# Kernel optimization log

Measured on AMD Instinct MI355X. Metric: run time of the kernel, lower is better.

The kernel has to match this reference:

```python
import jax, jax.numpy as jnp
import numpy as np

WORD_THRES = 0.2
COS_EPS = 1e-8
NEG_INF = -1e9


def setup_inputs() -> dict:
    key = jax.random.key(0)
    k1, k2, k3, k4 = jax.random.split(key, 4)
    B, L, V, E, A = 1024, 256, 50000, 300, 30
    inputs = jax.random.randint(k1, (B, L), 0, V)            # token ids, 0 == pad
    w_emb = jax.random.normal(k2, (V, E), dtype=jnp.float32) * 0.1
    a_emb = jax.random.normal(k3, (A, E), dtype=jnp.float32)
    a_weight = jax.random.uniform(k4, (A,), dtype=jnp.float32)
    return {"inputs": inputs, "w_emb": w_emb, "a_emb": a_emb, "a_weight": a_weight}


def reference(inputs, w_emb, a_emb, a_weight):
    # inputs: [B, L] int ids; w_emb: [V, E]; a_emb: [A, E]; a_weight: [A]
    inputs_len = (inputs != 0).sum(axis=1).astype(jnp.float32)      # [B]
    x_wrd = w_emb[inputs]                                            # [B, L, E]

    # cosine similarity between each aspect and each word (torch semantics:
    # dot / (max(||a||, eps) * max(||x||, eps)))
    a_norm = jnp.maximum(jnp.linalg.norm(a_emb, axis=-1), COS_EPS)   # [A]
    x_norm = jnp.maximum(jnp.linalg.norm(x_wrd, axis=-1), COS_EPS)   # [B, L]
    dot = jnp.einsum("ae,ble->abl", a_emb, x_wrd)                    # [A, B, L]
    sim = dot / (a_norm[:, None, None] * x_norm[None, :, :])

    # Threshold(word_thres, 0): x if x > thres else 0, then scale by aspect weight
    sim = jnp.where(sim > WORD_THRES, sim, 0.0) * a_weight[:, None, None]

    # centroid score: relu(sim).max over aspects, summed over seq, length-normalized
    centroid = jnp.maximum(sim, 0.0).max(axis=0)                     # [B, L]
    centroid_score = centroid.sum(axis=1) / (inputs_len + 1e-5)      # [B]

    # attention: mask exact zeros to -1e9, max over aspects, softmax over seq
    sim_m = jnp.where(sim == 0.0, NEG_INF, sim)
    scores = sim_m.max(axis=0)                                       # [B, L]
    a = jax.nn.softmax(scores, axis=1)                               # [B, L]

    z = jnp.einsum("bl,ble->be", a, x_wrd)                           # [B, E]
    enc_out = z * (centroid_score > 1e-4).astype(z.dtype)[:, None]
    return enc_out, a, centroid_score
```

## Files before the change

kernel.cpp:

```cpp
#include <hip/hip_runtime.h>
#include <math.h>

#define BB 1024
#define LL 256
#define VV 50000
#define EE 300
#define AA 30
#define WORD_THRES 0.2f
#define COS_EPS_F 1e-8f
#define NEG_INF_F -1e9f

__global__ void __launch_bounds__(256) cent_kernel(
    const float* __restrict__ w_emb,
    const float* __restrict__ a_emb,
    const float* __restrict__ a_weight,
    float* __restrict__ cent)
{
    __shared__ float4 s_a[AA * 75];
    __shared__ float s_scale[AA];
    __shared__ float s_aw[AA];

    const int t = threadIdx.x;
    const float4* __restrict__ a4 = (const float4*)a_emb;

    for (int s = t; s < AA * 75; s += 256) s_a[s] = a4[s];

    {
        const int a = t >> 3, j = t & 7;
        if (a < AA) {
            float n2a = 0.f;
            for (int c = j; c < 75; c += 8) {
                const float4 x = a4[a * 75 + c];
                n2a += x.x * x.x + x.y * x.y + x.z * x.z + x.w * x.w;
            }
            n2a += __shfl_xor(n2a, 1);
            n2a += __shfl_xor(n2a, 2);
            n2a += __shfl_xor(n2a, 4);
            if (j == 0) {
                s_scale[a] = 1.f / fmaxf(sqrtf(n2a), COS_EPS_F);
                s_aw[a] = a_weight[a];
            }
        }
    }
    __syncthreads();

    const int p = t & 3;
    const int slot = t >> 2;
    const int v0 = blockIdx.x * 128 + slot;
    const int v1 = v0 + 64;
    const bool ok1 = v1 < VV;
    const float* __restrict__ r0 = w_emb + (size_t)v0 * EE;
    const float* __restrict__ r1 = w_emb + (size_t)(ok1 ? v1 : 0) * EE;

    float acc0[AA], acc1[AA];
#pragma unroll
    for (int a = 0; a < AA; ++a) { acc0[a] = 0.f; acc1[a] = 0.f; }
    float n20 = 0.f, n21 = 0.f;

    for (int k = 0; k < 18; ++k) {
        const int j = 4 * k + p;
        const float4 w0 = *(const float4*)(r0 + 4 * j);
        const float4 w1 = *(const float4*)(r1 + 4 * j);
        n20 += w0.x * w0.x + w0.y * w0.y + w0.z * w0.z + w0.w * w0.w;
        n21 += w1.x * w1.x + w1.y * w1.y + w1.z * w1.z + w1.w * w1.w;
        const float4* __restrict__ ap = s_a + j;
#pragma unroll
        for (int a = 0; a < AA; ++a) {
            const float4 av = ap[a * 75];
            acc0[a] = fmaf(av.x, w0.x, fmaf(av.y, w0.y,
                      fmaf(av.z, w0.z, fmaf(av.w, w0.w, acc0[a]))));
            acc1[a] = fmaf(av.x, w1.x, fmaf(av.y, w1.y,
                      fmaf(av.z, w1.z, fmaf(av.w, w1.w, acc1[a]))));
        }
    }
    if (p < 3) {
        const int j = 72 + p;
        const float4 w0 = *(const float4*)(r0 + 4 * j);
        const float4 w1 = *(const float4*)(r1 + 4 * j);
        n20 += w0.x * w0.x + w0.y * w0.y + w0.z * w0.z + w0.w * w0.w;
        n21 += w1.x * w1.x + w1.y * w1.y + w1.z * w1.z + w1.w * w1.w;
        const float4* __restrict__ ap = s_a + j;
#pragma unroll
        for (int a = 0; a < AA; ++a) {
            const float4 av = ap[a * 75];
            acc0[a] = fmaf(av.x, w0.x, fmaf(av.y, w0.y,
                      fmaf(av.z, w0.z, fmaf(av.w, w0.w, acc0[a]))));
            acc1[a] = fmaf(av.x, w1.x, fmaf(av.y, w1.y,
                      fmaf(av.z, w1.z, fmaf(av.w, w1.w, acc1[a]))));
        }
    }

#pragma unroll
    for (int a = 0; a < AA; ++a) {
        acc0[a] += __shfl_xor(acc0[a], 1); acc0[a] += __shfl_xor(acc0[a], 2);
        acc1[a] += __shfl_xor(acc1[a], 1); acc1[a] += __shfl_xor(acc1[a], 2);
    }
    n20 += __shfl_xor(n20, 1); n20 += __shfl_xor(n20, 2);
    n21 += __shfl_xor(n21, 1); n21 += __shfl_xor(n21, 2);

    if (p == 0) {
        const float inv_x0 = 1.f / fmaxf(sqrtf(n20), COS_EPS_F);
        const float inv_x1 = 1.f / fmaxf(sqrtf(n21), COS_EPS_F);
        float m0 = 0.f, m1 = 0.f;
#pragma unroll
        for (int a = 0; a < AA; ++a) {
            const float c0 = acc0[a] * s_scale[a] * inv_x0;
            const float c1 = acc1[a] * s_scale[a] * inv_x1;
            m0 = fmaxf(m0, (c0 > WORD_THRES) ? c0 * s_aw[a] : 0.f);
            m1 = fmaxf(m1, (c1 > WORD_THRES) ? c1 * s_aw[a] : 0.f);
        }
        cent[v0] = m0;
        if (ok1) cent[v1] = m1;
    }
}

__global__ void __launch_bounds__(256) row_kernel(
    const int* __restrict__ inputs,
    const float* __restrict__ w_emb,
    const float* __restrict__ cent,
    float* __restrict__ out)
{
    const int b = blockIdx.x;
    const int t = threadIdx.x;
    const int wid = t >> 6, lane = t & 63;

    __shared__ float pA[4], pB[4], pC[4], pD[4];
    __shared__ int s_nact;
    __shared__ int s_act_id[LL];
    __shared__ float s_act_w[LL];

    const int id = inputs[b * LL + t];
    const float c = cent[id];
    const float score = (c > 0.f) ? c : NEG_INF_F;
    const float cnt = (id != 0) ? 1.f : 0.f;
    if (t == 0) s_nact = 0;

    float s1 = c, s2 = cnt, s3 = score;
#pragma unroll
    for (int o = 32; o > 0; o >>= 1) {
        s1 += __shfl_down(s1, o);
        s2 += __shfl_down(s2, o);
        s3 = fmaxf(s3, __shfl_down(s3, o));
    }
    if (lane == 0) { pA[wid] = s1; pB[wid] = s2; pC[wid] = s3; }
    __syncthreads();

    const float sum_c = pA[0] + pA[1] + pA[2] + pA[3];
    const float len   = pB[0] + pB[1] + pB[2] + pB[3];
    const float mx    = fmaxf(fmaxf(pC[0], pC[1]), fmaxf(pC[2], pC[3]));

    const float p = expf(score - mx);
    float s4 = p;
#pragma unroll
    for (int o = 32; o > 0; o >>= 1) s4 += __shfl_down(s4, o);
    if (lane == 0) pD[wid] = s4;
    __syncthreads();
    const float sum_p = pD[0] + pD[1] + pD[2] + pD[3];

    const float a_l = p / sum_p;
    const float cs = sum_c / (len + 1e-5f);
    const float gate = (cs > 1e-4f) ? 1.f : 0.f;

    out[BB * EE + b * LL + t] = a_l;
    if (t == 0) out[BB * EE + BB * LL + b] = cs;

    if (score > -1e8f) {
        const int i = atomicAdd(&s_nact, 1);
        s_act_id[i] = id;
        s_act_w[i] = a_l;
    }
    __syncthreads();
    const int n = s_nact;

    if (t < EE / 4) {
        float4 acc = {0.f, 0.f, 0.f, 0.f};
        for (int i = 0; i < n; ++i) {
            const float wgt = s_act_w[i];
            const float4 r = *(const float4*)(w_emb + (size_t)s_act_id[i] * EE + 4 * t);
            acc.x += wgt * r.x; acc.y += wgt * r.y;
            acc.z += wgt * r.z; acc.w += wgt * r.w;
        }
        acc.x *= gate; acc.y *= gate; acc.z *= gate; acc.w *= gate;
        *(float4*)(out + b * EE + 4 * t) = acc;
    }
}

extern "C" void kernel_launch(void* const* d_in, const int* in_sizes, int n_in,
                              void* d_out, int out_size, void* d_ws, size_t ws_size,
                              hipStream_t stream) {
    const int* inputs = (const int*)d_in[0];
    const float* w_emb = (const float*)d_in[1];
    const float* a_emb = (const float*)d_in[2];
    const float* a_weight = (const float*)d_in[3];
    float* out = (float*)d_out;
    float* cent = (float*)d_ws;

    cent_kernel<<<(VV + 127) / 128, 256, 0, stream>>>(w_emb, a_emb, a_weight, cent);
    row_kernel<<<BB, 256, 0, stream>>>(inputs, w_emb, cent, out);
}
```

Measured before the change: 126.6 us.

## Split aspect dimension across two grid blocks in centroid kernel

The per-vocabulary centroid kernel now launches a second grid dimension that divides the 30 aspects into two halves. Each block accumulates only 15 aspects and writes a partial max into its own slice of the workspace. The row kernel combines the two slices with a max. This halves the accumulator registers and shared memory per block and doubles the number of blocks, aiming for higher occupancy. In exchange, w_emb is read twice and the workspace needs twice the space.

```diff
diff --git a/kernel.cpp b/kernel.cpp
--- a/kernel.cpp
+++ b/kernel.cpp
@@ -6,6 +6,8 @@
 #define VV 50000
 #define EE 300
 #define AA 30
+#define ASPLIT 2
+#define APB (AA / ASPLIT)
 #define WORD_THRES 0.2f
 #define COS_EPS_F 1e-8f
 #define NEG_INF_F -1e9f
@@ -16,21 +18,22 @@
     const float* __restrict__ a_weight,
     float* __restrict__ cent)
 {
-    __shared__ float4 s_a[AA * 75];
-    __shared__ float s_scale[AA];
-    __shared__ float s_aw[AA];
+    __shared__ float4 s_a[APB * 75];
+    __shared__ float s_scale[APB];
+    __shared__ float s_aw[APB];
 
     const int t = threadIdx.x;
+    const int a0 = blockIdx.y * APB;
     const float4* __restrict__ a4 = (const float4*)a_emb;
 
-    for (int s = t; s < AA * 75; s += 256) s_a[s] = a4[s];
+    for (int s = t; s < APB * 75; s += 256) s_a[s] = a4[a0 * 75 + s];
 
     {
         const int a = t >> 3, j = t & 7;
-        if (a < AA) {
+        if (a < APB) {
             float n2a = 0.f;
             for (int c = j; c < 75; c += 8) {
-                const float4 x = a4[a * 75 + c];
+                const float4 x = a4[(a0 + a) * 75 + c];
                 n2a += x.x * x.x + x.y * x.y + x.z * x.z + x.w * x.w;
             }
             n2a += __shfl_xor(n2a, 1);
@@ -38,7 +41,7 @@
             n2a += __shfl_xor(n2a, 4);
             if (j == 0) {
                 s_scale[a] = 1.f / fmaxf(sqrtf(n2a), COS_EPS_F);
-                s_aw[a] = a_weight[a];
+                s_aw[a] = a_weight[a0 + a];
             }
         }
     }
@@ -52,9 +55,9 @@
     const float* __restrict__ r0 = w_emb + (size_t)v0 * EE;
     const float* __restrict__ r1 = w_emb + (size_t)(ok1 ? v1 : 0) * EE;
 
-    float acc0[AA], acc1[AA];
-#pragma unroll
-    for (int a = 0; a < AA; ++a) { acc0[a] = 0.f; acc1[a] = 0.f; }
+    float acc0[APB], acc1[APB];
+#pragma unroll
+    for (int a = 0; a < APB; ++a) { acc0[a] = 0.f; acc1[a] = 0.f; }
     float n20 = 0.f, n21 = 0.f;
 
     for (int k = 0; k < 18; ++k) {
@@ -65,7 +68,7 @@
         n21 += w1.x * w1.x + w1.y * w1.y + w1.z * w1.z + w1.w * w1.w;
         const float4* __restrict__ ap = s_a + j;
 #pragma unroll
-        for (int a = 0; a < AA; ++a) {
+        for (int a = 0; a < APB; ++a) {
             const float4 av = ap[a * 75];
             acc0[a] = fmaf(av.x, w0.x, fmaf(av.y, w0.y,
                       fmaf(av.z, w0.z, fmaf(av.w, w0.w, acc0[a]))));
@@ -81,7 +84,7 @@
         n21 += w1.x * w1.x + w1.y * w1.y + w1.z * w1.z + w1.w * w1.w;
         const float4* __restrict__ ap = s_a + j;
 #pragma unroll
-        for (int a = 0; a < AA; ++a) {
+        for (int a = 0; a < APB; ++a) {
             const float4 av = ap[a * 75];
             acc0[a] = fmaf(av.x, w0.x, fmaf(av.y, w0.y,
                       fmaf(av.z, w0.z, fmaf(av.w, w0.w, acc0[a]))));
@@ -91,7 +94,7 @@
     }
 
 #pragma unroll
-    for (int a = 0; a < AA; ++a) {
+    for (int a = 0; a < APB; ++a) {
         acc0[a] += __shfl_xor(acc0[a], 1); acc0[a] += __shfl_xor(acc0[a], 2);
         acc1[a] += __shfl_xor(acc1[a], 1); acc1[a] += __shfl_xor(acc1[a], 2);
     }
@@ -103,14 +106,15 @@
         const float inv_x1 = 1.f / fmaxf(sqrtf(n21), COS_EPS_F);
         float m0 = 0.f, m1 = 0.f;
 #pragma unroll
-        for (int a = 0; a < AA; ++a) {
+        for (int a = 0; a < APB; ++a) {
             const float c0 = acc0[a] * s_scale[a] * inv_x0;
             const float c1 = acc1[a] * s_scale[a] * inv_x1;
             m0 = fmaxf(m0, (c0 > WORD_THRES) ? c0 * s_aw[a] : 0.f);
             m1 = fmaxf(m1, (c1 > WORD_THRES) ? c1 * s_aw[a] : 0.f);
         }
-        cent[v0] = m0;
-        if (ok1) cent[v1] = m1;
+        float* __restrict__ ch = cent + (size_t)blockIdx.y * VV;
+        ch[v0] = m0;
+        if (ok1) ch[v1] = m1;
     }
 }
 
@@ -130,7 +134,7 @@
     __shared__ float s_act_w[LL];
 
     const int id = inputs[b * LL + t];
-    const float c = cent[id];
+    const float c = fmaxf(cent[id], cent[VV + id]);
     const float score = (c > 0.f) ? c : NEG_INF_F;
     const float cnt = (id != 0) ? 1.f : 0.f;
     if (t == 0) s_nact = 0;
@@ -195,6 +199,7 @@
     float* out = (float*)d_out;
     float* cent = (float*)d_ws;
 
-    cent_kernel<<<(VV + 127) / 128, 256, 0, stream>>>(w_emb, a_emb, a_weight, cent);
+    cent_kernel<<<dim3((VV + 127) / 128, ASPLIT), 256, 0, stream>>>(
+        w_emb, a_emb, a_weight, cent);
     row_kernel<<<BB, 256, 0, stream>>>(inputs, w_emb, cent, out);
 }
```

New measurement: 124.8 us. Within noise of the previous version (-1.4%).

## Compute vocab-aspect cosine dots with split-bf16 MFMA and threshold recheck

Applied to the files above, without the earlier changes.

Replaces the scalar FP32 FMA dot products in the per-vocabulary centroid kernel with 16x16x32 bf16 MFMA instructions. Each float is split into a bf16 high part and a bf16 low part, and three MFMA products approximate FP32 accuracy. Cosines that land near the threshold are recomputed exactly in FP32 so the thresholding decision stays correct. This removes the VALU-bound 30-aspect FMA loop, at the cost of conversion work, an extra LDS fragment layout and occasional divergent scalar rechecks.

```diff
diff --git a/kernel.cpp b/kernel.cpp
--- a/kernel.cpp
+++ b/kernel.cpp
@@ -9,6 +9,34 @@
 #define WORD_THRES 0.2f
 #define COS_EPS_F 1e-8f
 #define NEG_INF_F -1e9f
+#define RECHECK_DELTA 1e-3f
+
+typedef __attribute__((ext_vector_type(8))) short bf16x8;
+typedef __attribute__((ext_vector_type(4))) float f32x4;
+
+#define MFMA16(a, b, c) __builtin_amdgcn_mfma_f32_16x16x32_bf16((a), (b), (c), 0, 0, 0)
+
+__device__ __forceinline__ unsigned pack_hi(float a, float b) {
+    return (__float_as_uint(a) >> 16) | (__float_as_uint(b) & 0xFFFF0000u);
+}
+__device__ __forceinline__ float hi_part(float a) {
+    return __uint_as_float(__float_as_uint(a) & 0xFFFF0000u);
+}
+__device__ __forceinline__ void cvt_hilo(const float4 f0, const float4 f1,
+                                         uint4& uh, uint4& ul) {
+    uh.x = pack_hi(f0.x, f0.y);
+    uh.y = pack_hi(f0.z, f0.w);
+    uh.z = pack_hi(f1.x, f1.y);
+    uh.w = pack_hi(f1.z, f1.w);
+    const float l0 = f0.x - hi_part(f0.x), l1 = f0.y - hi_part(f0.y);
+    const float l2 = f0.z - hi_part(f0.z), l3 = f0.w - hi_part(f0.w);
+    const float l4 = f1.x - hi_part(f1.x), l5 = f1.y - hi_part(f1.y);
+    const float l6 = f1.z - hi_part(f1.z), l7 = f1.w - hi_part(f1.w);
+    ul.x = pack_hi(l0, l1);
+    ul.y = pack_hi(l2, l3);
+    ul.z = pack_hi(l4, l5);
+    ul.w = pack_hi(l6, l7);
+}
 
 __global__ void __launch_bounds__(256) cent_kernel(
     const float* __restrict__ w_emb,
@@ -16,21 +44,23 @@
     const float* __restrict__ a_weight,
     float* __restrict__ cent)
 {
-    __shared__ float4 s_a[AA * 75];
-    __shared__ float s_scale[AA];
-    __shared__ float s_aw[AA];
+    __shared__ uint4 s_bfrag[40 * 64];
+    __shared__ float s_scale[32];
+    __shared__ float s_aw[32];
 
     const int t = threadIdx.x;
-    const float4* __restrict__ a4 = (const float4*)a_emb;
-
-    for (int s = t; s < AA * 75; s += 256) s_a[s] = a4[s];
+    const int l = t & 63;
+    const int w = t >> 6;
+    const int m = l & 15;
+    const int kg = l >> 4;
 
     {
         const int a = t >> 3, j = t & 7;
         if (a < AA) {
+            const float4* a4 = (const float4*)a_emb + a * 75;
             float n2a = 0.f;
             for (int c = j; c < 75; c += 8) {
-                const float4 x = a4[a * 75 + c];
+                const float4 x = a4[c];
                 n2a += x.x * x.x + x.y * x.y + x.z * x.z + x.w * x.w;
             }
             n2a += __shfl_xor(n2a, 1);
@@ -41,76 +71,126 @@
                 s_aw[a] = a_weight[a];
             }
         }
-    }
-    __syncthreads();
-
-    const int p = t & 3;
-    const int slot = t >> 2;
-    const int v0 = blockIdx.x * 128 + slot;
-    const int v1 = v0 + 64;
-    const bool ok1 = v1 < VV;
-    const float* __restrict__ r0 = w_emb + (size_t)v0 * EE;
-    const float* __restrict__ r1 = w_emb + (size_t)(ok1 ? v1 : 0) * EE;
-
-    float acc0[AA], acc1[AA];
-#pragma unroll
-    for (int a = 0; a < AA; ++a) { acc0[a] = 0.f; acc1[a] = 0.f; }
-    float n20 = 0.f, n21 = 0.f;
-
-    for (int k = 0; k < 18; ++k) {
-        const int j = 4 * k + p;
-        const float4 w0 = *(const float4*)(r0 + 4 * j);
-        const float4 w1 = *(const float4*)(r1 + 4 * j);
-        n20 += w0.x * w0.x + w0.y * w0.y + w0.z * w0.z + w0.w * w0.w;
-        n21 += w1.x * w1.x + w1.y * w1.y + w1.z * w1.z + w1.w * w1.w;
-        const float4* __restrict__ ap = s_a + j;
-#pragma unroll
-        for (int a = 0; a < AA; ++a) {
-            const float4 av = ap[a * 75];
-            acc0[a] = fmaf(av.x, w0.x, fmaf(av.y, w0.y,
-                      fmaf(av.z, w0.z, fmaf(av.w, w0.w, acc0[a]))));
-            acc1[a] = fmaf(av.x, w1.x, fmaf(av.y, w1.y,
-                      fmaf(av.z, w1.z, fmaf(av.w, w1.w, acc1[a]))));
-        }
-    }
-    if (p < 3) {
-        const int j = 72 + p;
-        const float4 w0 = *(const float4*)(r0 + 4 * j);
-        const float4 w1 = *(const float4*)(r1 + 4 * j);
-        n20 += w0.x * w0.x + w0.y * w0.y + w0.z * w0.z + w0.w * w0.w;
-        n21 += w1.x * w1.x + w1.y * w1.y + w1.z * w1.z + w1.w * w1.w;
-        const float4* __restrict__ ap = s_a + j;
-#pragma unroll
-        for (int a = 0; a < AA; ++a) {
-            const float4 av = ap[a * 75];
-            acc0[a] = fmaf(av.x, w0.x, fmaf(av.y, w0.y,
-                      fmaf(av.z, w0.z, fmaf(av.w, w0.w, acc0[a]))));
-            acc1[a] = fmaf(av.x, w1.x, fmaf(av.y, w1.y,
-                      fmaf(av.z, w1.z, fmaf(av.w, w1.w, acc1[a]))));
-        }
-    }
-
-#pragma unroll
-    for (int a = 0; a < AA; ++a) {
-        acc0[a] += __shfl_xor(acc0[a], 1); acc0[a] += __shfl_xor(acc0[a], 2);
-        acc1[a] += __shfl_xor(acc1[a], 1); acc1[a] += __shfl_xor(acc1[a], 2);
-    }
-    n20 += __shfl_xor(n20, 1); n20 += __shfl_xor(n20, 2);
-    n21 += __shfl_xor(n21, 1); n21 += __shfl_xor(n21, 2);
-
-    if (p == 0) {
-        const float inv_x0 = 1.f / fmaxf(sqrtf(n20), COS_EPS_F);
-        const float inv_x1 = 1.f / fmaxf(sqrtf(n21), COS_EPS_F);
-        float m0 = 0.f, m1 = 0.f;
-#pragma unroll
-        for (int a = 0; a < AA; ++a) {
-            const float c0 = acc0[a] * s_scale[a] * inv_x0;
-            const float c1 = acc1[a] * s_scale[a] * inv_x1;
-            m0 = fmaxf(m0, (c0 > WORD_THRES) ? c0 * s_aw[a] : 0.f);
-            m1 = fmaxf(m1, (c1 > WORD_THRES) ? c1 * s_aw[a] : 0.f);
-        }
-        cent[v0] = m0;
-        if (ok1) cent[v1] = m1;
+        if (t == 30 || t == 31) { s_scale[t] = 0.f; s_aw[t] = 0.f; }
+    }
+
+    for (int ks = w; ks < 10; ks += 4) {
+        const int kb = kg * 8 + 32 * ks;
+#pragma unroll
+        for (int tt = 0; tt < 2; ++tt) {
+            const int col = tt * 16 + m;
+            float4 f0 = {0.f, 0.f, 0.f, 0.f}, f1 = {0.f, 0.f, 0.f, 0.f};
+            if (col < AA) {
+                const float* ap = a_emb + col * EE;
+                if (kb <= 296) f0 = *(const float4*)(ap + kb);
+                if (kb <= 292) f1 = *(const float4*)(ap + kb + 4);
+            }
+            uint4 uh, ul;
+            cvt_hilo(f0, f1, uh, ul);
+            s_bfrag[(ks * 4 + tt * 2 + 0) * 64 + l] = uh;
+            s_bfrag[(ks * 4 + tt * 2 + 1) * 64 + l] = ul;
+        }
+    }
+    __syncthreads();
+
+    const int vbase = blockIdx.x * 64 + w * 16;
+    const int v = vbase + m;
+    const float* __restrict__ rowp = w_emb + (size_t)((v < VV) ? v : 0) * EE;
+
+    f32x4 acc0 = {0.f, 0.f, 0.f, 0.f};
+    f32x4 acc1 = {0.f, 0.f, 0.f, 0.f};
+    float n2 = 0.f;
+    const uint4* __restrict__ bp0 = s_bfrag + l;
+
+#pragma unroll 3
+    for (int ks = 0; ks < 9; ++ks) {
+        const int kb = kg * 8 + 32 * ks;
+        const float4 f0 = *(const float4*)(rowp + kb);
+        const float4 f1 = *(const float4*)(rowp + kb + 4);
+        n2 = fmaf(f0.x, f0.x, fmaf(f0.y, f0.y, fmaf(f0.z, f0.z, fmaf(f0.w, f0.w, n2))));
+        n2 = fmaf(f1.x, f1.x, fmaf(f1.y, f1.y, fmaf(f1.z, f1.z, fmaf(f1.w, f1.w, n2))));
+        uint4 uh, ul;
+        cvt_hilo(f0, f1, uh, ul);
+        const bf16x8 ah = __builtin_bit_cast(bf16x8, uh);
+        const bf16x8 al = __builtin_bit_cast(bf16x8, ul);
+        const uint4* bp = bp0 + ks * 256;
+        const bf16x8 bh0 = __builtin_bit_cast(bf16x8, bp[0]);
+        const bf16x8 bl0 = __builtin_bit_cast(bf16x8, bp[64]);
+        const bf16x8 bh1 = __builtin_bit_cast(bf16x8, bp[128]);
+        const bf16x8 bl1 = __builtin_bit_cast(bf16x8, bp[192]);
+        acc0 = MFMA16(ah, bh0, acc0);
+        acc1 = MFMA16(ah, bh1, acc1);
+        acc0 = MFMA16(ah, bl0, acc0);
+        acc1 = MFMA16(ah, bl1, acc1);
+        acc0 = MFMA16(al, bh0, acc0);
+        acc1 = MFMA16(al, bh1, acc1);
+    }
+    {
+        const int kb = kg * 8 + 288;
+        float4 f0 = {0.f, 0.f, 0.f, 0.f}, f1 = {0.f, 0.f, 0.f, 0.f};
+        if (kb <= 296) f0 = *(const float4*)(rowp + kb);
+        if (kb <= 292) f1 = *(const float4*)(rowp + kb + 4);
+        n2 = fmaf(f0.x, f0.x, fmaf(f0.y, f0.y, fmaf(f0.z, f0.z, fmaf(f0.w, f0.w, n2))));
+        n2 = fmaf(f1.x, f1.x, fmaf(f1.y, f1.y, fmaf(f1.z, f1.z, fmaf(f1.w, f1.w, n2))));
+        uint4 uh, ul;
+        cvt_hilo(f0, f1, uh, ul);
+        const bf16x8 ah = __builtin_bit_cast(bf16x8, uh);
+        const bf16x8 al = __builtin_bit_cast(bf16x8, ul);
+        const uint4* bp = bp0 + 9 * 256;
+        const bf16x8 bh0 = __builtin_bit_cast(bf16x8, bp[0]);
+        const bf16x8 bl0 = __builtin_bit_cast(bf16x8, bp[64]);
+        const bf16x8 bh1 = __builtin_bit_cast(bf16x8, bp[128]);
+        const bf16x8 bl1 = __builtin_bit_cast(bf16x8, bp[192]);
+        acc0 = MFMA16(ah, bh0, acc0);
+        acc1 = MFMA16(ah, bh1, acc1);
+        acc0 = MFMA16(ah, bl0, acc0);
+        acc1 = MFMA16(ah, bl1, acc1);
+        acc0 = MFMA16(al, bh0, acc0);
+        acc1 = MFMA16(al, bh1, acc1);
+    }
+
+    n2 += __shfl_xor(n2, 16);
+    n2 += __shfl_xor(n2, 32);
+
+    const float sc0 = s_scale[m], aw0 = s_aw[m];
+    const float sc1 = s_scale[16 + m], aw1 = s_aw[16 + m];
+    const bool col1ok = (16 + m) < AA;
+    float mx[4];
+#pragma unroll
+    for (int j = 0; j < 4; ++j) {
+        const int r = kg * 4 + j;
+        const float n2r = __int_as_float(
+            __builtin_amdgcn_ds_bpermute(r << 2, __float_as_int(n2)));
+        const float inv_x = 1.f / fmaxf(sqrtf(n2r), COS_EPS_F);
+        float c0 = acc0[j] * sc0 * inv_x;
+        float c1 = acc1[j] * sc1 * inv_x;
+        if (fabsf(c0 - WORD_THRES) < RECHECK_DELTA) {
+            const int rr = vbase + r;
+            const float* wr = w_emb + (size_t)((rr < VV) ? rr : 0) * EE;
+            const float* ar = a_emb + m * EE;
+            float d = 0.f;
+            for (int k = 0; k < EE; ++k) d = fmaf(wr[k], ar[k], d);
+            c0 = d * sc0 * inv_x;
+        }
+        if (col1ok && fabsf(c1 - WORD_THRES) < RECHECK_DELTA) {
+            const int rr = vbase + r;
+            const float* wr = w_emb + (size_t)((rr < VV) ? rr : 0) * EE;
+            const float* ar = a_emb + (16 + m) * EE;
+            float d = 0.f;
+            for (int k = 0; k < EE; ++k) d = fmaf(wr[k], ar[k], d);
+            c1 = d * sc1 * inv_x;
+        }
+        float mj = fmaxf((c0 > WORD_THRES) ? c0 * aw0 : 0.f,
+                         (c1 > WORD_THRES) ? c1 * aw1 : 0.f);
+        mj = fmaxf(mj, __shfl_xor(mj, 1));
+        mj = fmaxf(mj, __shfl_xor(mj, 2));
+        mj = fmaxf(mj, __shfl_xor(mj, 4));
+        mj = fmaxf(mj, __shfl_xor(mj, 8));
+        mx[j] = mj;
+    }
+    if (m == 0 && vbase < VV) {
+        const float4 o = {mx[0], mx[1], mx[2], mx[3]};
+        *(float4*)(cent + vbase + kg * 4) = o;
     }
 }
 
@@ -195,6 +275,6 @@
     float* out = (float*)d_out;
     float* cent = (float*)d_ws;
 
-    cent_kernel<<<(VV + 127) / 128, 256, 0, stream>>>(w_emb, a_emb, a_weight, cent);
+    cent_kernel<<<(VV + 63) / 64, 256, 0, stream>>>(w_emb, a_emb, a_weight, cent);
     row_kernel<<<BB, 256, 0, stream>>>(inputs, w_emb, cent, out);
 }
```

After: 114.4 us. 9.6% less time.
